# Optimization experiments

Hardware: AMD Instinct MI355X
Metric: run time of the kernel (lower is better)

The kernel has to match this reference:

```python
import jax, jax.numpy as jnp
import numpy as np

BIG = 1e30
B, Hh, Ww, DM = 8, 64, 64, 128
DI = 2 * DM          # d_inner
RR = -(-DM // 16)    # dt_rank = ceil(DM/16)
HID = 512


def _ln(x, g, b, eps):
    mu = jnp.mean(x, -1, keepdims=True)
    var = jnp.mean((x - mu) ** 2, -1, keepdims=True)
    return (x - mu) * jax.lax.rsqrt(var + eps) * g + b


def _silu(x):
    return x * jax.nn.sigmoid(x)


def _grid_weights(f):
    # f: [D,H,W]; MST edge weights exp(-cosine_sim) on 4-connected grid, BIG = invalid
    def cos(a, b):
        num = jnp.sum(a * b, 0)
        den = jnp.maximum(jnp.linalg.norm(a, axis=0) * jnp.linalg.norm(b, axis=0), 1e-8)
        return num / den
    wr = jnp.pad(jnp.exp(-cos(f[:, :, :-1], f[:, :, 1:])), ((0, 0), (0, 1)), constant_values=BIG).reshape(-1)
    wd = jnp.pad(jnp.exp(-cos(f[:, :-1, :], f[:, 1:, :])), ((0, 1), (0, 0)), constant_values=BIG).reshape(-1)
    return wr, wd


def _mst(wr, wd, H, W):
    # Prim's minimum spanning tree on HxW grid. Addition order is a valid
    # topological order (parent precedes child), equivalent to the BFS sort
    # for the order-invariant tree-scan aggregation.
    L = H * W

    def body(t, st):
        dist, par, intree, order = st
        v = jnp.argmin(jnp.where(intree, BIG, dist)).astype(jnp.int32)
        intree = intree.at[v].set(True)
        order = order.at[t].set(v)
        r, c = v // W, v % W
        for u, valid, w in (
            (v + 1, c < W - 1, wr[v]),
            (v - 1, c > 0, wr[jnp.clip(v - 1, 0, L - 1)]),
            (v + W, r < H - 1, wd[v]),
            (v - W, r > 0, wd[jnp.clip(v - W, 0, L - 1)]),
        ):
            uc = jnp.clip(u, 0, L - 1)
            better = valid & (~intree[uc]) & (w < dist[uc])
            dist = dist.at[uc].set(jnp.where(better, w, dist[uc]))
            par = par.at[uc].set(jnp.where(better, v, par[uc]))
        return dist, par, intree, order

    st0 = (jnp.full((L,), BIG, jnp.float32).at[0].set(-1.0),
           jnp.zeros((L,), jnp.int32),
           jnp.zeros((L,), bool),
           jnp.zeros((L,), jnp.int32))
    _, par, _, order = jax.lax.fori_loop(0, L, body, st0)
    return order, par


def _tree_scan(feat, ew, order, par):
    # feat, ew: [D,L]. Two-pass tree filter: out[i] = sum_j prod_{e in path(i,j)} w_e * f[j]
    vs = order[1:]
    ps = par[vs]

    def up_step(up, vp):
        v, p = vp
        return up.at[:, p].add(ew[:, v] * up[:, v]), None

    up, _ = jax.lax.scan(up_step, feat, (vs[::-1], ps[::-1]))
    root = order[0]
    out0 = jnp.zeros_like(up).at[:, root].set(up[:, root])

    def down_step(out, vp):
        v, p = vp
        w = ew[:, v]
        return out.at[:, v].set(up[:, v] + w * (out[:, p] - w * up[:, v])), None

    out, _ = jax.lax.scan(down_step, out0, (vs, ps))
    return out


def reference(x, ln1_g, ln1_b, ln2_g, ln2_b, w_in, conv_w, x_weight, dt_weight,
              dt_bias, a_logs, ds, hn_g, hn_b, on_g, on_b, w_out,
              mlp_w1, mlp_b1, mlp_w2, mlp_b2):
    Bb, H, W, _ = x.shape
    L = H * W
    # --- TreeScan branch ---
    h = _ln(x, ln1_g, ln1_b, 1e-6)
    xc, z = jnp.split(h @ w_in.T, 2, -1)
    z = _silu(z)
    xc = jnp.transpose(xc, (0, 3, 1, 2))                      # [B,Di,H,W]
    xc = _silu(jax.lax.conv_general_dilated(
        xc, conv_w, (1, 1), ((1, 1), (1, 1)),
        dimension_numbers=('NCHW', 'OIHW', 'NCHW'),
        feature_group_count=xc.shape[1]))
    Di = xc.shape[1]
    xs = xc.reshape(Bb, Di, L)
    R = dt_weight.shape[2]
    x_dbl = jnp.einsum('bdl,cd->bcl', xs, x_weight[0])        # [B,R+2,L]
    dts, Bs, Cs = x_dbl[:, :R], x_dbl[:, R:R + 1], x_dbl[:, R + 1:]
    dts = jnp.einsum('brl,dr->bdl', dts, dt_weight[0])
    dts = jax.nn.softplus(dts + dt_bias.reshape(-1)[None, :, None])
    As = -jnp.exp(a_logs.reshape(-1).astype(jnp.float32))     # N=1
    deltaA = jnp.exp(dts * As[None, :, None])                 # per-channel edge weights
    feat_in = dts * Bs * xs                                   # deltaB * x (K=N=1)
    # MST + topological sort under no-grad (matches torch.no_grad())
    f4t = jax.lax.stop_gradient(xs).reshape(Bb, Di, H, W)
    wr, wd = jax.vmap(_grid_weights)(f4t)
    order, par = jax.vmap(lambda a, b: _mst(a, b, H, W))(wr, wd)
    feat_out = jax.vmap(_tree_scan)(feat_in, deltaA, order, par)  # [B,Di,L]
    ho = _ln(jnp.swapaxes(feat_out, 1, 2), hn_g, hn_b, 1e-5)      # h_norm
    y = jnp.swapaxes(ho * jnp.swapaxes(Cs, 1, 2), 1, 2)           # multiply by Cs (N=1)
    y = y + ds[None, :, None] * xs                                # D skip
    y = _ln(jnp.swapaxes(y, 1, 2), on_g, on_b, 1e-5).reshape(Bb, H, W, Di)
    scan_out = (y * z) @ w_out.T
    # --- residual + MLP ---
    x1 = x + scan_out
    h2 = _ln(x1, ln2_g, ln2_b, 1e-6)
    mlp = jax.nn.gelu(h2 @ mlp_w1.T + mlp_b1) @ mlp_w2.T + mlp_b2
    return x1 + mlp


def setup_inputs():
    key = jax.random.key(0)
    ks = jax.random.split(key, 12)

    def rn(k, shape, s):
        return jax.random.normal(k, shape, jnp.float32) * s

    dt = jnp.exp(jax.random.uniform(ks[10], (DI,)) * (np.log(0.1) - np.log(0.001)) + np.log(0.001))
    dt_bias = (dt + jnp.log(-jnp.expm1(-dt)))[None]  # inverse-softplus init
    return {
        'x': rn(ks[0], (B, Hh, Ww, DM), 1.0),
        'ln1_g': jnp.ones((DM,)), 'ln1_b': jnp.zeros((DM,)),
        'ln2_g': jnp.ones((DM,)), 'ln2_b': jnp.zeros((DM,)),
        'w_in': rn(ks[1], (2 * DI, DM), DM ** -0.5),
        'conv_w': rn(ks[2], (DI, 1, 3, 3), 1.0 / 3.0),
        'x_weight': rn(ks[3], (1, RR + 2, DI), DI ** -0.5),
        'dt_weight': rn(ks[4], (1, DI, RR), RR ** -0.5),
        'dt_bias': dt_bias,
        'a_logs': jnp.zeros((DI, 1)),
        'ds': jnp.ones((DI,)),
        'hn_g': jnp.ones((DI,)), 'hn_b': jnp.zeros((DI,)),
        'on_g': jnp.ones((DI,)), 'on_b': jnp.zeros((DI,)),
        'w_out': rn(ks[5], (DM, DI), DI ** -0.5),
        'mlp_w1': rn(ks[6], (HID, DM), DM ** -0.5),
        'mlp_b1': jnp.zeros((HID,)),
        'mlp_w2': rn(ks[7], (DM, HID), HID ** -0.5),
        'mlp_b2': jnp.zeros((DM,)),
    }
```

## Files before the change

### kernel.cpp

```cpp
#include <hip/hip_runtime.h>
#include <hip/hip_bf16.h>
#include <cstdint>

#define BIGF 1e30f
constexpr int LB   = 4096;
constexpr int NB   = 8;
constexpr int MROWS = NB * LB;
constexpr int LSP  = 4104;

__device__ __forceinline__ float warp_sum(float v) {
#pragma unroll
  for (int off = 32; off; off >>= 1) v += __shfl_xor(v, off);
  return v;
}

__device__ __forceinline__ float block_sum256(float v) {
  __shared__ float sm[4];
  v = warp_sum(v);
  __syncthreads();
  if ((threadIdx.x & 63) == 0) sm[threadIdx.x >> 6] = v;
  __syncthreads();
  return sm[0] + sm[1] + sm[2] + sm[3];
}

__global__ __launch_bounds__(256) void ln128_kernel(
    const float* __restrict__ X, const float* __restrict__ g,
    const float* __restrict__ bb, float* __restrict__ O, float eps) {
  int wave = threadIdx.x >> 6, lane = threadIdx.x & 63;
  int row = blockIdx.x * 4 + wave;
  const float* xr = X + (size_t)row * 128;
  float x0 = xr[lane], x1 = xr[lane + 64];
  float mu = warp_sum(x0 + x1) * (1.0f / 128.0f);
  float d0 = x0 - mu, d1 = x1 - mu;
  float var = warp_sum(d0 * d0 + d1 * d1) * (1.0f / 128.0f);
  float s = 1.0f / sqrtf(var + eps);
  float* orow = O + (size_t)row * 128;
  orow[lane]      = d0 * s * g[lane]      + bb[lane];
  orow[lane + 64] = d1 * s * g[lane + 64] + bb[lane + 64];
}

template<int EPI>
__global__ __launch_bounds__(256) void gemm_kernel(
    const float* __restrict__ A, const float* __restrict__ W,
    float* __restrict__ C, float* __restrict__ C2,
    const float* __restrict__ bias, const float* __restrict__ addsrc,
    int M, int N, int K) {
  __shared__ float As[32][68];
  __shared__ float Bs[32][68];
  int t = threadIdx.x;
  int tx = t & 15, ty = t >> 4;
  int bm = blockIdx.y * 64, bn = blockIdx.x * 64;
  float acc[4][4] = {};
  for (int k0 = 0; k0 < K; k0 += 32) {
#pragma unroll
    for (int hh = 0; hh < 2; ++hh) {
      int q = t + hh * 256;
      int r = q >> 3, kc = q & 7;
      float4 a4 = reinterpret_cast<const float4*>(A + (size_t)(bm + r) * K + k0)[kc];
      float4 b4 = reinterpret_cast<const float4*>(W + (size_t)(bn + r) * K + k0)[kc];
      As[kc * 4 + 0][r] = a4.x; As[kc * 4 + 1][r] = a4.y;
      As[kc * 4 + 2][r] = a4.z; As[kc * 4 + 3][r] = a4.w;
      Bs[kc * 4 + 0][r] = b4.x; Bs[kc * 4 + 1][r] = b4.y;
      Bs[kc * 4 + 2][r] = b4.z; Bs[kc * 4 + 3][r] = b4.w;
    }
    __syncthreads();
#pragma unroll
    for (int kk = 0; kk < 32; ++kk) {
      float4 av = *reinterpret_cast<const float4*>(&As[kk][ty * 4]);
      float4 bv = *reinterpret_cast<const float4*>(&Bs[kk][tx * 4]);
      float aa[4] = {av.x, av.y, av.z, av.w};
      float bbv[4] = {bv.x, bv.y, bv.z, bv.w};
#pragma unroll
      for (int i = 0; i < 4; ++i)
#pragma unroll
        for (int j = 0; j < 4; ++j) acc[i][j] += aa[i] * bbv[j];
    }
    __syncthreads();
  }
#pragma unroll
  for (int i = 0; i < 4; ++i) {
    int m = bm + ty * 4 + i;
#pragma unroll
    for (int j = 0; j < 4; ++j) {
      int n = bn + tx * 4 + j;
      float v = acc[i][j];
      if (EPI == 1) {
        if (n < 256) C[(size_t)m * 256 + n] = v;
        else C2[(size_t)m * 256 + (n - 256)] = v / (1.0f + expf(-v));
      } else if (EPI == 2) {
        C[(size_t)m * N + n] = v + addsrc[(size_t)m * N + n];
      } else if (EPI == 3) {
        float u = v + bias[n];
        C[(size_t)m * N + n] =
            0.5f * u * (1.0f + tanhf(0.7978845608028654f * (u + 0.044715f * u * u * u)));
      } else if (EPI == 4) {
        C[(size_t)m * N + n] = v + bias[n] + addsrc[(size_t)m * N + n];
      }
    }
  }
}

__global__ __launch_bounds__(256) void convfeat_kernel(
    const float* __restrict__ xcpre, const float* __restrict__ cw,
    const float* __restrict__ xw, const float* __restrict__ dtw,
    const float* __restrict__ dtb, const float* __restrict__ alogs,
    float* __restrict__ xs, float* __restrict__ dAt, float* __restrict__ featt,
    float* __restrict__ Cs, float* __restrict__ ssq) {
  int m = blockIdx.x;
  int d = threadIdx.x;
  int l = m & (LB - 1), b = m >> 12;
  int r = l >> 6, c = l & 63;
  float acc = 0.f;
#pragma unroll
  for (int ky = 0; ky < 3; ++ky) {
    int rr = r + ky - 1;
    if (rr < 0 || rr > 63) continue;
#pragma unroll
    for (int kx = 0; kx < 3; ++kx) {
      int cc = c + kx - 1;
      if (cc < 0 || cc > 63) continue;
      int ml = (b << 12) + (rr << 6) + cc;
      acc += xcpre[(size_t)ml * 256 + d] * cw[d * 9 + ky * 3 + kx];
    }
  }
  float xv = acc / (1.0f + expf(-acc));
  xs[(size_t)m * 256 + d] = xv;
  float p[11];
#pragma unroll
  for (int i = 0; i < 10; ++i) p[i] = xv * xw[i * 256 + d];
  p[10] = xv * xv;
  __shared__ float sm[4][11];
#pragma unroll
  for (int i = 0; i < 11; ++i) p[i] = warp_sum(p[i]);
  int wv = d >> 6;
  if ((d & 63) == 0) {
    for (int i = 0; i < 11; ++i) sm[wv][i] = p[i];
  }
  __syncthreads();
  float red[11];
#pragma unroll
  for (int i = 0; i < 11; ++i) red[i] = sm[0][i] + sm[1][i] + sm[2][i] + sm[3][i];
  float xdt = dtb[d];
#pragma unroll
  for (int rr2 = 0; rr2 < 8; ++rr2) xdt += red[rr2] * dtw[d * 8 + rr2];
  float sp = fmaxf(xdt, 0.f) + log1pf(expf(-fabsf(xdt)));
  float As_ = -expf(alogs[d]);
  size_t tidx = ((size_t)(b * 64 + (d >> 2)) * 4096 + l) * 4 + (d & 3);
  dAt[tidx]   = expf(sp * As_);
  featt[tidx] = sp * red[8] * xv;
  if (d == 0) { Cs[m] = red[9]; ssq[m] = red[10]; }
}

__global__ __launch_bounds__(256) void gridw_kernel(
    const float* __restrict__ xs, const float* __restrict__ ssq,
    float* __restrict__ wrg, float* __restrict__ wdg) {
  int m = blockIdx.x, d = threadIdx.x;
  int l = m & (LB - 1);
  int r = l >> 6, c = l & 63;
  float a = xs[(size_t)m * 256 + d];
  float br = (c < 63) ? xs[(size_t)(m + 1) * 256 + d] : 0.f;
  float bd = (r < 63) ? xs[(size_t)(m + 64) * 256 + d] : 0.f;
  float s1 = warp_sum(a * br);
  float s2 = warp_sum(a * bd);
  __shared__ float sm[4][2];
  int wv = d >> 6;
  if ((d & 63) == 0) { sm[wv][0] = s1; sm[wv][1] = s2; }
  __syncthreads();
  if (d == 0) {
    float dotr = sm[0][0] + sm[1][0] + sm[2][0] + sm[3][0];
    float dotd = sm[0][1] + sm[1][1] + sm[2][1] + sm[3][1];
    float na = sqrtf(ssq[m]);
    float wrv = BIGF, wdv = BIGF;
    if (c < 63) { float den = fmaxf(na * sqrtf(ssq[m + 1]), 1e-8f);  wrv = expf(-(dotr / den)); }
    if (r < 63) { float den = fmaxf(na * sqrtf(ssq[m + 64]), 1e-8f); wdv = expf(-(dotd / den)); }
    wrg[m] = wrv; wdg[m] = wdv;
  }
}

__global__ __launch_bounds__(1024) void mst_kernel(
    const float* __restrict__ wr_g, const float* __restrict__ wd_g,
    unsigned short* __restrict__ levn16_g, unsigned short* __restrict__ parn16_g,
    int* __restrict__ levs_g) {
  __shared__ int pool[24592];
  __shared__ unsigned char flagR[4096];
  __shared__ unsigned char flagD[4096];
  __shared__ int ncomp_s;
  __shared__ int wred[16];
  int b = blockIdx.x, tid = threadIdx.x;
  float* wrs = (float*)pool;
  float* wds = (float*)(pool + 4096);
  int* comp = pool + 8192;
  int* lnk  = pool + 12288;
  unsigned int* bestw = (unsigned int*)(pool + 16384);
  int* beste = pool + 20480;
  const float* wrb = wr_g + b * 4096;
  const float* wdb = wd_g + b * 4096;
  for (int k = 0; k < 4; ++k) {
    int i = tid + k * 1024;
    wrs[i] = wrb[i]; wds[i] = wdb[i];
    comp[i] = i; flagR[i] = 0; flagD[i] = 0;
  }
  __syncthreads();
  for (int phase = 0; phase < 13; ++phase) {
    for (int k = 0; k < 4; ++k) {
      int c = tid + k * 1024;
      bestw[c] = 0xFFFFFFFFu; beste[c] = 0x7FFFFFFF; lnk[c] = c;
    }
    if (tid == 0) ncomp_s = 0;
    __syncthreads();
    for (int k = 0; k < 8; ++k) {
      int e = tid + k * 1024;
      int v = e & 4095;
      bool isR = e < 4096;
      int c = v & 63, r = v >> 6;
      bool valid = isR ? (c < 63) : (r < 63);
      if (valid) {
        int u = isR ? v + 1 : v + 64;
        int ca = comp[v], cb = comp[u];
        if (ca != cb) {
          unsigned wbits = __float_as_uint(isR ? wrs[v] : wds[v]);
          atomicMin(&bestw[ca], wbits);
          atomicMin(&bestw[cb], wbits);
        }
      }
    }
    __syncthreads();
    for (int k = 0; k < 8; ++k) {
      int e = tid + k * 1024;
      int v = e & 4095;
      bool isR = e < 4096;
      int c = v & 63, r = v >> 6;
      bool valid = isR ? (c < 63) : (r < 63);
      if (valid) {
        int u = isR ? v + 1 : v + 64;
        int ca = comp[v], cb = comp[u];
        if (ca != cb) {
          unsigned wbits = __float_as_uint(isR ? wrs[v] : wds[v]);
          if (wbits == bestw[ca]) atomicMin(&beste[ca], e);
          if (wbits == bestw[cb]) atomicMin(&beste[cb], e);
        }
      }
    }
    __syncthreads();
    for (int k = 0; k < 4; ++k) {
      int cc = tid + k * 1024;
      int e = beste[cc];
      if (e != 0x7FFFFFFF) {
        int v = e & 4095;
        bool isR = e < 4096;
        int u = isR ? v + 1 : v + 64;
        if (isR) flagR[v] = 1; else flagD[v] = 1;
        int ca = comp[v], cb = comp[u];
        lnk[cc] = (ca == cc) ? cb : ca;
      }
    }
    __syncthreads();
    for (int k = 0; k < 4; ++k) {
      int cc = tid + k * 1024;
      int l = lnk[cc];
      if (l != cc && lnk[l] == cc && cc < l) lnk[cc] = cc;
    }
    __syncthreads();
    for (int it = 0; it < 12; ++it) {
      for (int k = 0; k < 4; ++k) {
        int cc = tid + k * 1024;
        lnk[cc] = lnk[lnk[cc]];
      }
      __syncthreads();
    }
    for (int k = 0; k < 4; ++k) {
      int i = tid + k * 1024;
      comp[i] = lnk[comp[i]];
      if (comp[i] == i) atomicAdd(&ncomp_s, 1);
    }
    __syncthreads();
    if (ncomp_s <= 1) break;
    __syncthreads();
  }
  unsigned short* nxt = (unsigned short*)pool;
  short*          dsv = (short*)(pool + 8200);
  int* par = pool + 16400;
  int* dep = pool + 20496;
  const int NIL = 16384;
  unsigned short rn[16];
  int rd[16];
  int validm = 0;
  for (int k = 0; k < 4; ++k) { int i = tid + k * 1024; par[i] = 0; dep[i] = 0; }
#pragma unroll
  for (int k = 0; k < 16; ++k) {
    int a = tid + k * 1024;
    int u = a >> 2, d = a & 3;
    int c = u & 63, r = u >> 6;
    int mu = 0;
    if (r > 0  && flagD[u - 64]) mu |= 1;
    if (c > 0  && flagR[u - 1])  mu |= 2;
    if (c < 63 && flagR[u])      mu |= 4;
    if (r < 63 && flagD[u])      mu |= 8;
    unsigned short nx = NIL; short dv = 0;
    if (mu & (1 << d)) {
      validm |= 1 << k;
      int v = u + ((d == 0) ? -64 : (d == 1) ? -1 : (d == 2) ? 1 : 64);
      int cv = v & 63, rv = v >> 6;
      int mv = 0;
      if (rv > 0  && flagD[v - 64]) mv |= 1;
      if (cv > 0  && flagR[v - 1])  mv |= 2;
      if (cv < 63 && flagR[v])      mv |= 4;
      if (rv < 63 && flagD[v])      mv |= 8;
      int din = 3 - d;
      int hi = mv >> (din + 1);
      int dn = hi ? (din + __ffs(hi)) : (__ffs(mv) - 1);
      int nxv = v * 4 + dn;
      int m0 = (flagR[0] ? 4 : 0) | (flagD[0] ? 8 : 0);
      int a0 = __ffs(m0) - 1;
      if (v == 0 && nxv == a0) nxv = NIL;
      nx = (unsigned short)nxv;
      dv = 1;
    }
    nxt[a] = nx; dsv[a] = dv;
    rn[k] = nx; rd[k] = dv;
  }
  if (tid == 0) { nxt[NIL] = NIL; dsv[NIL] = 0; }
  __syncthreads();
#pragma unroll 1
  for (int it = 0; it < 13; ++it) {
    unsigned short nn[16]; short nd[16];
#pragma unroll
    for (int k = 0; k < 16; ++k) { nn[k] = nxt[rn[k]]; nd[k] = dsv[rn[k]]; }
    __syncthreads();
#pragma unroll
    for (int k = 0; k < 16; ++k) {
      int a = tid + k * 1024;
      rd[k] += nd[k];
      rn[k] = nn[k];
      nxt[a] = rn[k]; dsv[a] = (short)rd[k];
    }
    __syncthreads();
  }
#pragma unroll
  for (int k = 0; k < 16; ++k) if (validm & (1 << k)) {
    int a = tid + k * 1024;
    int u = a >> 2, d = a & 3;
    int v = u + ((d == 0) ? -64 : (d == 1) ? -1 : (d == 2) ? 1 : 64);
    int rb = v * 4 + (3 - d);
    if (rd[k] > (int)dsv[rb]) par[v] = u;
  }
  __syncthreads();
#pragma unroll
  for (int k = 0; k < 16; ++k) {
    int a = tid + k * 1024;
    int u = a >> 2, d = a & 3;
    unsigned short nx = NIL; short dv = 0;
    if (validm & (1 << k)) {
      int v = u + ((d == 0) ? -64 : (d == 1) ? -1 : (d == 2) ? 1 : 64);
      int cv = v & 63, rv = v >> 6;
      int mv = 0;
      if (rv > 0  && flagD[v - 64]) mv |= 1;
      if (cv > 0  && flagR[v - 1])  mv |= 2;
      if (cv < 63 && flagR[v])      mv |= 4;
      if (rv < 63 && flagD[v])      mv |= 8;
      int din = 3 - d;
      int hi = mv >> (din + 1);
      int dn = hi ? (din + __ffs(hi)) : (__ffs(mv) - 1);
      int nxv = v * 4 + dn;
      int m0 = (flagR[0] ? 4 : 0) | (flagD[0] ? 8 : 0);
      int a0 = __ffs(m0) - 1;
      if (v == 0 && nxv == a0) nxv = NIL;
      nx = (unsigned short)nxv;
      dv = (par[v] == u) ? (short)1 : (short)-1;
    }
    nxt[a] = nx; dsv[a] = dv;
    rn[k] = nx; rd[k] = dv;
  }
  __syncthreads();
#pragma unroll 1
  for (int it = 0; it < 13; ++it) {
    unsigned short nn[16]; short nd[16];
#pragma unroll
    for (int k = 0; k < 16; ++k) { nn[k] = nxt[rn[k]]; nd[k] = dsv[rn[k]]; }
    __syncthreads();
#pragma unroll
    for (int k = 0; k < 16; ++k) {
      int a = tid + k * 1024;
      rd[k] += nd[k];
      rn[k] = nn[k];
      nxt[a] = rn[k]; dsv[a] = (short)rd[k];
    }
    __syncthreads();
  }
#pragma unroll
  for (int k = 0; k < 16; ++k) if (validm & (1 << k)) {
    int a = tid + k * 1024;
    int u = a >> 2, d = a & 3;
    int v = u + ((d == 0) ? -64 : (d == 1) ? -1 : (d == 2) ? 1 : 64);
    if (par[v] == u) dep[v] = 1 - rd[k];
  }
  __syncthreads();
  int md = 0;
  for (int k = 0; k < 4; ++k) md = max(md, dep[tid + k * 1024]);
#pragma unroll
  for (int off = 32; off; off >>= 1) md = max(md, __shfl_xor(md, off));
  if ((tid & 63) == 0) wred[tid >> 6] = md;
  __syncthreads();
  if (tid == 0) {
    int m = 0;
    for (int i = 0; i < 16; ++i) m = max(m, wred[i]);
    wred[0] = m;
  }
  __syncthreads();
  int maxd = wred[0];
  __syncthreads();
  int* cnt  = pool;
  int* offs = pool + 4096;
  for (int k = 0; k < 4; ++k) cnt[tid + k * 1024] = 0;
  __syncthreads();
  for (int k = 0; k < 4; ++k) atomicAdd(&cnt[dep[tid + k * 1024]], 1);
  __syncthreads();
  int base4 = tid * 4;
  int c0 = cnt[base4], c1 = cnt[base4 + 1], c2 = cnt[base4 + 2], c3 = cnt[base4 + 3];
  int tsum = c0 + c1 + c2 + c3;
  int lane = tid & 63, wid = tid >> 6;
  int iv = tsum;
  for (int off = 1; off < 64; off <<= 1) {
    int n = __shfl_up(iv, off);
    if (lane >= off) iv += n;
  }
  if (lane == 63) wred[wid] = iv;
  __syncthreads();
  if (tid == 0) {
    int acc = 0;
    for (int i = 0; i < 16; ++i) { int t = wred[i]; wred[i] = acc; acc += t; }
  }
  __syncthreads();
  int excl = iv - tsum + wred[wid];
  offs[base4]     = excl;
  offs[base4 + 1] = excl + c0;
  offs[base4 + 2] = excl + c0 + c1;
  offs[base4 + 3] = excl + c0 + c1 + c2;
  __syncthreads();
  for (int idx = tid; idx <= maxd; idx += 1024) levs_g[b * LSP + idx] = offs[idx];
  if (tid == 0) {
    levs_g[b * LSP + maxd + 1] = 4096;
    levs_g[b * LSP + 4098] = maxd + 1;
  }
  __syncthreads();
  for (int k = 0; k < 4; ++k) {
    int v2 = tid + k * 1024;
    int pos = atomicAdd(&offs[dep[v2]], 1);
    int c = v2 & 63, r = v2 >> 6;
    unsigned msk = 0;
    if (r > 0  && par[v2 - 64] == v2) msk |= 1;
    if (c > 0  && par[v2 - 1]  == v2) msk |= 2;
    if (c < 63 && par[v2 + 1]  == v2) msk |= 4;
    if (r < 63 && par[v2 + 64] == v2) msk |= 8;
    levn16_g[b * 4096 + pos] = (unsigned short)(v2 | (msk << 12));
    parn16_g[b * 4096 + pos] = (unsigned short)par[v2];
  }
}

__global__ __launch_bounds__(64) void scan_kernel(
    float* __restrict__ buft, const float* __restrict__ ewt,
    const unsigned short* __restrict__ levn16_g,
    const unsigned short* __restrict__ parn16_g,
    const int* __restrict__ levs_g) {
  __shared__ float pr[32776];
  __shared__ unsigned int topo[4096];
  __shared__ unsigned short lvs[4104];
  int bid = blockIdx.x;
  int b = bid >> 6;
  int cg = bid & 63;
  int lane = threadIdx.x;
  int nlev = levs_g[b * LSP + 4098];
  size_t tbase = (size_t)(b * 64 + cg) * 4096;
  float2* pr2 = reinterpret_cast<float2*>(pr);
  const float4* bt4 = reinterpret_cast<const float4*>(buft) + tbase;
  const float4* et4 = reinterpret_cast<const float4*>(ewt) + tbase;
  for (int n = lane; n < 4096; n += 64) {
    float4 bv = bt4[n];
    float4 ev = et4[n];
    pr2[0 * 4097 + n] = make_float2(bv.x, ev.x);
    pr2[1 * 4097 + n] = make_float2(bv.y, ev.y);
    pr2[2 * 4097 + n] = make_float2(bv.z, ev.z);
    pr2[3 * 4097 + n] = make_float2(bv.w, ev.w);
  }
  const unsigned int* lv32 = reinterpret_cast<const unsigned int*>(levn16_g + b * 4096);
  const unsigned int* pn32 = reinterpret_cast<const unsigned int*>(parn16_g + b * 4096);
  for (int i2 = lane; i2 < 2048; i2 += 64) {
    unsigned int a = lv32[i2], p = pn32[i2];
    topo[2 * i2]     = (a & 0xFFFFu) | (p << 16);
    topo[2 * i2 + 1] = (a >> 16) | (p & 0xFFFF0000u);
  }
  for (int i = lane; i <= nlev; i += 64) lvs[i] = (unsigned short)levs_g[b * LSP + i];
  __syncthreads();
  int ch = lane & 3;
  int slot = lane >> 2;
  int cpl = ch * 4097;
  if (nlev > 1) {
    int s = lvs[nlev - 1], e = lvs[nlev];
    int jn = s + slot;
    unsigned int pkn = topo[jn & 4095];
    for (int lev = nlev - 1; lev >= 1; --lev) {
      int ce = e;
      int j = jn;
      unsigned int pk = pkn;
      if (lev > 1) {
        e = s; s = lvs[lev - 1];
        jn = s + slot;
        pkn = topo[jn & 4095];
      }
      bool first = true;
      while (j < ce) {
        if (!first) pk = topo[j];
        first = false;
        int v = pk & 4095;
        int p = (pk >> 16) & 4095;
        float2 self = pr2[cpl + v];
        atomicAdd(&pr[(cpl + p) * 2], self.y * self.x);
        j += 16;
      }
      __builtin_amdgcn_wave_barrier();
    }
  }
  __builtin_amdgcn_wave_barrier();
  if (nlev > 1) {
    int s = lvs[1], e = lvs[2];
    int jn = s + slot;
    unsigned int pkn = topo[jn & 4095];
    for (int lev = 1; lev < nlev; ++lev) {
      int ce = e;
      int j = jn;
      unsigned int pk = pkn;
      if (lev + 1 < nlev) {
        s = e; e = lvs[lev + 2];
        jn = s + slot;
        pkn = topo[jn & 4095];
      }
      bool first = true;
      while (j < ce) {
        if (!first) pk = topo[j];
        first = false;
        int v = pk & 4095;
        int p = (pk >> 16) & 4095;
        float2 self = pr2[cpl + v];
        float pb = pr[(cpl + p) * 2];
        float w = self.y, uv = self.x;
        pr[(cpl + v) * 2] = uv + w * (pb - w * uv);
        j += 16;
      }
      __builtin_amdgcn_wave_barrier();
    }
  }
  __syncthreads();
  float4* bw4 = reinterpret_cast<float4*>(buft) + tbase;
  for (int n = lane; n < 4096; n += 64) {
    float2 c0 = pr2[0 * 4097 + n];
    float2 c1 = pr2[1 * 4097 + n];
    float2 c2 = pr2[2 * 4097 + n];
    float2 c3 = pr2[3 * 4097 + n];
    bw4[n] = make_float4(c0.x, c1.x, c2.x, c3.x);
  }
}

__global__ __launch_bounds__(256) void post_kernel(
    const float* __restrict__ buft, const float* __restrict__ Cs,
    const float* __restrict__ xs, const float* __restrict__ ds,
    const float* __restrict__ hng, const float* __restrict__ hnb,
    const float* __restrict__ ong, const float* __restrict__ onb,
    float* __restrict__ zya) {
  int m = blockIdx.x, d = threadIdx.x;
  int b = m >> 12, l = m & (LB - 1);
  size_t idx = (size_t)m * 256 + d;
  float fo = buft[((size_t)(b * 64 + (d >> 2)) * 4096 + l) * 4 + (d & 3)];
  float mu = block_sum256(fo) * (1.f / 256.f);
  float dv = fo - mu;
  float var = block_sum256(dv * dv) * (1.f / 256.f);
  float ho = dv * (1.0f / sqrtf(var + 1e-5f)) * hng[d] + hnb[d];
  float y = ho * Cs[m] + ds[d] * xs[idx];
  float mu2 = block_sum256(y) * (1.f / 256.f);
  float dy = y - mu2;
  float var2 = block_sum256(dy * dy) * (1.f / 256.f);
  float y2 = dy * (1.0f / sqrtf(var2 + 1e-5f)) * ong[d] + onb[d];
  zya[idx] = y2 * zya[idx];
}

extern "C" void kernel_launch(void* const* d_in, const int* in_sizes, int n_in,
                              void* d_out, int out_size, void* d_ws, size_t ws_size,
                              hipStream_t stream) {
  (void)in_sizes; (void)n_in; (void)out_size; (void)ws_size;
  const float* x      = (const float*)d_in[0];
  const float* ln1g   = (const float*)d_in[1];
  const float* ln1b   = (const float*)d_in[2];
  const float* ln2g   = (const float*)d_in[3];
  const float* ln2b   = (const float*)d_in[4];
  const float* w_in   = (const float*)d_in[5];
  const float* conv_w = (const float*)d_in[6];
  const float* xw     = (const float*)d_in[7];
  const float* dtw    = (const float*)d_in[8];
  const float* dtb    = (const float*)d_in[9];
  const float* alogs  = (const float*)d_in[10];
  const float* dsv    = (const float*)d_in[11];
  const float* hng    = (const float*)d_in[12];
  const float* hnb    = (const float*)d_in[13];
  const float* ong    = (const float*)d_in[14];
  const float* onb    = (const float*)d_in[15];
  const float* w_out  = (const float*)d_in[16];
  const float* mw1    = (const float*)d_in[17];
  const float* mb1    = (const float*)d_in[18];
  const float* mw2    = (const float*)d_in[19];
  const float* mb2    = (const float*)d_in[20];

  char* ws = (char*)d_ws;
  float* h    = (float*)(ws + 0);
  float* z    = (float*)(ws + 16777216);
  float* xcp  = (float*)(ws + 50331648);
  float* xs   = (float*)(ws + 83886080);
  float* dAt  = (float*)(ws + 117440512);
  float* featt= (float*)(ws + 150994944);
  float* Cs   = (float*)(ws + 184549376);
  float* ssq  = (float*)(ws + 184680448);
  float* wr   = (float*)(ws + 184811520);
  float* wd   = (float*)(ws + 184942592);
  unsigned short* levn16 = (unsigned short*)(ws + 185073664);
  unsigned short* parn16 = (unsigned short*)(ws + 185204736);
  int*   levs = (int*)(ws + 185335808);
  float* midg = xs;
  float* x1   = h;
  float* h2   = xcp;

  ln128_kernel<<<MROWS / 4, 256, 0, stream>>>(x, ln1g, ln1b, h, 1e-6f);
  gemm_kernel<1><<<dim3(8, 512), 256, 0, stream>>>(h, w_in, xcp, z, nullptr, nullptr,
                                                   MROWS, 512, 128);
  convfeat_kernel<<<MROWS, 256, 0, stream>>>(xcp, conv_w, xw, dtw, dtb, alogs,
                                             xs, dAt, featt, Cs, ssq);
  gridw_kernel<<<MROWS, 256, 0, stream>>>(xs, ssq, wr, wd);
  mst_kernel<<<NB, 1024, 0, stream>>>(wr, wd, levn16, parn16, levs);
  scan_kernel<<<512, 64, 0, stream>>>(featt, dAt, levn16, parn16, levs);
  post_kernel<<<MROWS, 256, 0, stream>>>(featt, Cs, xs, dsv, hng, hnb, ong, onb, z);
  gemm_kernel<2><<<dim3(2, 512), 256, 0, stream>>>(z, w_out, x1, nullptr, nullptr, x,
                                                   MROWS, 128, 256);
  ln128_kernel<<<MROWS / 4, 256, 0, stream>>>(x1, ln2g, ln2b, h2, 1e-6f);
  gemm_kernel<3><<<dim3(8, 512), 256, 0, stream>>>(h2, mw1, midg, nullptr, mb1, nullptr,
                                                   MROWS, 512, 128);
  gemm_kernel<4><<<dim3(2, 512), 256, 0, stream>>>(midg, mw2, (float*)d_out, nullptr,
                                                   mb2, x1, MROWS, 128, 512);
}
```

Measured before the change: 874.4 us.

## Add 128x128 GEMM tile, fast-math intrinsics, packed topo, and restructured tree scan

Result: faster. 841.0 us (-3.8%).

```diff
diff --git a/kernel.cpp b/kernel.cpp
--- a/kernel.cpp
+++ b/kernel.cpp
@@ -84,17 +84,68 @@
     for (int j = 0; j < 4; ++j) {
       int n = bn + tx * 4 + j;
       float v = acc[i][j];
+      if (EPI == 2) {
+        C[(size_t)m * N + n] = v + addsrc[(size_t)m * N + n];
+      } else if (EPI == 4) {
+        C[(size_t)m * N + n] = v + bias[n] + addsrc[(size_t)m * N + n];
+      }
+    }
+  }
+}
+
+template<int EPI>
+__global__ __launch_bounds__(256) void gemm128_kernel(
+    const float* __restrict__ A, const float* __restrict__ W,
+    float* __restrict__ C, float* __restrict__ C2,
+    const float* __restrict__ bias, int M, int N, int K) {
+  __shared__ float As[32][132];
+  __shared__ float Bs[32][132];
+  int t = threadIdx.x;
+  int tx = t & 15, ty = t >> 4;
+  int bm = blockIdx.y * 128, bn = blockIdx.x * 128;
+  float acc[8][8] = {};
+  for (int k0 = 0; k0 < K; k0 += 32) {
+#pragma unroll
+    for (int hh = 0; hh < 4; ++hh) {
+      int q = t + hh * 256;
+      int r = q >> 3, kc = q & 7;
+      float4 a4 = *reinterpret_cast<const float4*>(A + (size_t)(bm + r) * K + k0 + kc * 4);
+      float4 b4 = *reinterpret_cast<const float4*>(W + (size_t)(bn + r) * K + k0 + kc * 4);
+      As[kc * 4 + 0][r] = a4.x; As[kc * 4 + 1][r] = a4.y;
+      As[kc * 4 + 2][r] = a4.z; As[kc * 4 + 3][r] = a4.w;
+      Bs[kc * 4 + 0][r] = b4.x; Bs[kc * 4 + 1][r] = b4.y;
+      Bs[kc * 4 + 2][r] = b4.z; Bs[kc * 4 + 3][r] = b4.w;
+    }
+    __syncthreads();
+#pragma unroll
+    for (int kk = 0; kk < 32; ++kk) {
+      float4 a0 = *reinterpret_cast<const float4*>(&As[kk][ty * 4]);
+      float4 a1 = *reinterpret_cast<const float4*>(&As[kk][64 + ty * 4]);
+      float4 b0 = *reinterpret_cast<const float4*>(&Bs[kk][tx * 4]);
+      float4 b1 = *reinterpret_cast<const float4*>(&Bs[kk][64 + tx * 4]);
+      float aa[8] = {a0.x, a0.y, a0.z, a0.w, a1.x, a1.y, a1.z, a1.w};
+      float bb2[8] = {b0.x, b0.y, b0.z, b0.w, b1.x, b1.y, b1.z, b1.w};
+#pragma unroll
+      for (int i = 0; i < 8; ++i)
+#pragma unroll
+        for (int j = 0; j < 8; ++j) acc[i][j] += aa[i] * bb2[j];
+    }
+    __syncthreads();
+  }
+#pragma unroll
+  for (int i = 0; i < 8; ++i) {
+    int m = bm + (i >> 2) * 64 + ty * 4 + (i & 3);
+#pragma unroll
+    for (int j = 0; j < 8; ++j) {
+      int n = bn + (j >> 2) * 64 + tx * 4 + (j & 3);
+      float v = acc[i][j];
       if (EPI == 1) {
         if (n < 256) C[(size_t)m * 256 + n] = v;
-        else C2[(size_t)m * 256 + (n - 256)] = v / (1.0f + expf(-v));
-      } else if (EPI == 2) {
-        C[(size_t)m * N + n] = v + addsrc[(size_t)m * N + n];
+        else C2[(size_t)m * 256 + (n - 256)] = v / (1.0f + __expf(-v));
       } else if (EPI == 3) {
         float u = v + bias[n];
-        C[(size_t)m * N + n] =
-            0.5f * u * (1.0f + tanhf(0.7978845608028654f * (u + 0.044715f * u * u * u)));
-      } else if (EPI == 4) {
-        C[(size_t)m * N + n] = v + bias[n] + addsrc[(size_t)m * N + n];
+        float xg = 1.5957691216057308f * (u + 0.044715f * u * u * u);
+        C[(size_t)m * N + n] = u / (1.0f + __expf(-xg));
       }
     }
   }
@@ -123,7 +174,7 @@
       acc += xcpre[(size_t)ml * 256 + d] * cw[d * 9 + ky * 3 + kx];
     }
   }
-  float xv = acc / (1.0f + expf(-acc));
+  float xv = acc / (1.0f + __expf(-acc));
   xs[(size_t)m * 256 + d] = xv;
   float p[11];
 #pragma unroll
@@ -143,10 +194,10 @@
   float xdt = dtb[d];
 #pragma unroll
   for (int rr2 = 0; rr2 < 8; ++rr2) xdt += red[rr2] * dtw[d * 8 + rr2];
-  float sp = fmaxf(xdt, 0.f) + log1pf(expf(-fabsf(xdt)));
-  float As_ = -expf(alogs[d]);
+  float sp = fmaxf(xdt, 0.f) + __logf(1.0f + __expf(-fabsf(xdt)));
+  float As_ = -__expf(alogs[d]);
   size_t tidx = ((size_t)(b * 64 + (d >> 2)) * 4096 + l) * 4 + (d & 3);
-  dAt[tidx]   = expf(sp * As_);
+  dAt[tidx]   = __expf(sp * As_);
   featt[tidx] = sp * red[8] * xv;
   if (d == 0) { Cs[m] = red[9]; ssq[m] = red[10]; }
 }
@@ -179,8 +230,7 @@
 
 __global__ __launch_bounds__(1024) void mst_kernel(
     const float* __restrict__ wr_g, const float* __restrict__ wd_g,
-    unsigned short* __restrict__ levn16_g, unsigned short* __restrict__ parn16_g,
-    int* __restrict__ levs_g) {
+    unsigned int* __restrict__ topo_g, int* __restrict__ levs_g) {
   __shared__ int pool[24592];
   __shared__ unsigned char flagR[4096];
   __shared__ unsigned char flagD[4096];
@@ -452,112 +502,109 @@
     if (c > 0  && par[v2 - 1]  == v2) msk |= 2;
     if (c < 63 && par[v2 + 1]  == v2) msk |= 4;
     if (r < 63 && par[v2 + 64] == v2) msk |= 8;
-    levn16_g[b * 4096 + pos] = (unsigned short)(v2 | (msk << 12));
-    parn16_g[b * 4096 + pos] = (unsigned short)par[v2];
+    topo_g[b * 4096 + pos] =
+        (unsigned)v2 | (msk << 12) | ((unsigned)par[v2] << 16);
   }
 }
 
 __global__ __launch_bounds__(64) void scan_kernel(
     float* __restrict__ buft, const float* __restrict__ ewt,
-    const unsigned short* __restrict__ levn16_g,
-    const unsigned short* __restrict__ parn16_g,
-    const int* __restrict__ levs_g) {
-  __shared__ float pr[32776];
-  __shared__ unsigned int topo[4096];
+    const unsigned int* __restrict__ topo_g, const int* __restrict__ levs_g) {
+  __shared__ float acc[16384];
   __shared__ unsigned short lvs[4104];
   int bid = blockIdx.x;
-  int b = bid >> 6;
-  int cg = bid & 63;
+  int b = bid >> 6, cg = bid & 63;
   int lane = threadIdx.x;
+  int ch = lane & 3, slot = lane >> 2;
   int nlev = levs_g[b * LSP + 4098];
-  size_t tbase = (size_t)(b * 64 + cg) * 4096;
-  float2* pr2 = reinterpret_cast<float2*>(pr);
-  const float4* bt4 = reinterpret_cast<const float4*>(buft) + tbase;
-  const float4* et4 = reinterpret_cast<const float4*>(ewt) + tbase;
+  size_t fbase = (size_t)(b * 64 + cg) * 16384;
+  const float4* bt4 = reinterpret_cast<const float4*>(buft + fbase);
+  const float*  ewf = ewt + fbase;
+  const float4* et4 = reinterpret_cast<const float4*>(ewf);
+  const unsigned int* tp = topo_g + b * 4096;
+  float4* acc4 = reinterpret_cast<float4*>(acc);
+  float wsum = 0.f;
   for (int n = lane; n < 4096; n += 64) {
-    float4 bv = bt4[n];
+    acc4[n] = bt4[n];
     float4 ev = et4[n];
-    pr2[0 * 4097 + n] = make_float2(bv.x, ev.x);
-    pr2[1 * 4097 + n] = make_float2(bv.y, ev.y);
-    pr2[2 * 4097 + n] = make_float2(bv.z, ev.z);
-    pr2[3 * 4097 + n] = make_float2(bv.w, ev.w);
-  }
-  const unsigned int* lv32 = reinterpret_cast<const unsigned int*>(levn16_g + b * 4096);
-  const unsigned int* pn32 = reinterpret_cast<const unsigned int*>(parn16_g + b * 4096);
-  for (int i2 = lane; i2 < 2048; i2 += 64) {
-    unsigned int a = lv32[i2], p = pn32[i2];
-    topo[2 * i2]     = (a & 0xFFFFu) | (p << 16);
-    topo[2 * i2 + 1] = (a >> 16) | (p & 0xFFFF0000u);
-  }
+    wsum += ev.x + ev.y + ev.z + ev.w;
+  }
+  asm volatile("" :: "v"(wsum));
   for (int i = lane; i <= nlev; i += 64) lvs[i] = (unsigned short)levs_g[b * LSP + i];
   __syncthreads();
-  int ch = lane & 3;
-  int slot = lane >> 2;
-  int cpl = ch * 4097;
   if (nlev > 1) {
-    int s = lvs[nlev - 1], e = lvs[nlev];
-    int jn = s + slot;
-    unsigned int pkn = topo[jn & 4095];
+    int sA = lvs[nlev - 1], eA = lvs[nlev];
+    int jA = sA + slot;
+    unsigned tAv = tp[jA < 4096 ? jA : 4095];
+    int vA = tAv & 4095, pA = (tAv >> 16) & 4095;
+    float elA = ewf[vA * 4 + ch];
+    int sB = 0, eB = 0, jB = 0; unsigned tBv = 0;
+    if (nlev - 2 >= 1) { sB = lvs[nlev - 2]; eB = sA; jB = sB + slot; tBv = tp[jB < 4096 ? jB : 4095]; }
     for (int lev = nlev - 1; lev >= 1; --lev) {
-      int ce = e;
-      int j = jn;
-      unsigned int pk = pkn;
-      if (lev > 1) {
-        e = s; s = lvs[lev - 1];
-        jn = s + slot;
-        pkn = topo[jn & 4095];
-      }
-      bool first = true;
-      while (j < ce) {
-        if (!first) pk = topo[j];
-        first = false;
-        int v = pk & 4095;
-        int p = (pk >> 16) & 4095;
-        float2 self = pr2[cpl + v];
-        atomicAdd(&pr[(cpl + p) * 2], self.y * self.x);
-        j += 16;
+      int vB = tBv & 4095, pB = (tBv >> 16) & 4095;
+      float elB = 0.f;
+      if (lev - 1 >= 1) elB = ewf[vB * 4 + ch];
+      int sC = 0, jC = 0; unsigned tCv = 0;
+      if (lev - 2 >= 1) { sC = lvs[lev - 2]; jC = sC + slot; tCv = tp[jC < 4096 ? jC : 4095]; }
+      if (jA < eA) {
+        float a = acc[vA * 4 + ch];
+        atomicAdd(&acc[pA * 4 + ch], elA * a);
+        for (int j = jA + 16; j < eA; j += 16) {
+          unsigned t = tp[j];
+          int v = t & 4095, p = (t >> 16) & 4095;
+          float e = ewf[v * 4 + ch];
+          float av = acc[v * 4 + ch];
+          atomicAdd(&acc[p * 4 + ch], e * av);
+        }
       }
       __builtin_amdgcn_wave_barrier();
+      int oldsB = sB;
+      vA = vB; pA = pB; elA = elB; jA = jB; eA = eB; sA = oldsB;
+      sB = sC; eB = oldsB; jB = jC; tBv = tCv;
     }
   }
   __builtin_amdgcn_wave_barrier();
   if (nlev > 1) {
-    int s = lvs[1], e = lvs[2];
-    int jn = s + slot;
-    unsigned int pkn = topo[jn & 4095];
+    int sA = lvs[1], eA = lvs[2];
+    int jA = sA + slot;
+    unsigned tAv = tp[jA < 4096 ? jA : 4095];
+    int vA = tAv & 4095, pA = (tAv >> 16) & 4095;
+    float elA = ewf[vA * 4 + ch];
+    float uvA = acc[vA * 4 + ch];
+    int sB = 0, eB = 0, jB = 0; unsigned tBv = 0;
+    if (nlev > 2) { sB = eA; eB = lvs[3 <= nlev ? 3 : nlev]; jB = sB + slot; tBv = tp[jB < 4096 ? jB : 4095]; }
     for (int lev = 1; lev < nlev; ++lev) {
-      int ce = e;
-      int j = jn;
-      unsigned int pk = pkn;
+      int vB = tBv & 4095, pB = (tBv >> 16) & 4095;
+      float elB = 0.f, uvB = 0.f;
       if (lev + 1 < nlev) {
-        s = e; e = lvs[lev + 2];
-        jn = s + slot;
-        pkn = topo[jn & 4095];
-      }
-      bool first = true;
-      while (j < ce) {
-        if (!first) pk = topo[j];
-        first = false;
-        int v = pk & 4095;
-        int p = (pk >> 16) & 4095;
-        float2 self = pr2[cpl + v];
-        float pb = pr[(cpl + p) * 2];
-        float w = self.y, uv = self.x;
-        pr[(cpl + v) * 2] = uv + w * (pb - w * uv);
-        j += 16;
+        elB = ewf[vB * 4 + ch];
+        uvB = acc[vB * 4 + ch];
+      }
+      int sC = 0, eC = 0, jC = 0; unsigned tCv = 0;
+      if (lev + 2 < nlev) {
+        sC = lvs[lev + 2]; eC = lvs[lev + 3];
+        jC = sC + slot; tCv = tp[jC < 4096 ? jC : 4095];
+      }
+      if (jA < eA) {
+        float pb = acc[pA * 4 + ch];
+        acc[vA * 4 + ch] = uvA + elA * (pb - elA * uvA);
+        for (int j = jA + 16; j < eA; j += 16) {
+          unsigned t = tp[j];
+          int v = t & 4095, p = (t >> 16) & 4095;
+          float e = ewf[v * 4 + ch];
+          float uv = acc[v * 4 + ch];
+          float pbv = acc[p * 4 + ch];
+          acc[v * 4 + ch] = uv + e * (pbv - e * uv);
+        }
       }
       __builtin_amdgcn_wave_barrier();
-    }
-  }
-  __syncthreads();
-  float4* bw4 = reinterpret_cast<float4*>(buft) + tbase;
-  for (int n = lane; n < 4096; n += 64) {
-    float2 c0 = pr2[0 * 4097 + n];
-    float2 c1 = pr2[1 * 4097 + n];
-    float2 c2 = pr2[2 * 4097 + n];
-    float2 c3 = pr2[3 * 4097 + n];
-    bw4[n] = make_float4(c0.x, c1.x, c2.x, c3.x);
-  }
+      vA = vB; pA = pB; elA = elB; uvA = uvB; jA = jB; sA = sB; eA = eB;
+      sB = sC; eB = eC; jB = jC; tBv = tCv;
+    }
+  }
+  __syncthreads();
+  float4* bw4 = reinterpret_cast<float4*>(buft + fbase);
+  for (int n = lane; n < 4096; n += 64) bw4[n] = acc4[n];
 }
 
 __global__ __launch_bounds__(256) void post_kernel(
@@ -619,27 +666,26 @@
   float* ssq  = (float*)(ws + 184680448);
   float* wr   = (float*)(ws + 184811520);
   float* wd   = (float*)(ws + 184942592);
-  unsigned short* levn16 = (unsigned short*)(ws + 185073664);
-  unsigned short* parn16 = (unsigned short*)(ws + 185204736);
+  unsigned int* topo32 = (unsigned int*)(ws + 185073664);
   int*   levs = (int*)(ws + 185335808);
   float* midg = xs;
   float* x1   = h;
   float* h2   = xcp;
 
   ln128_kernel<<<MROWS / 4, 256, 0, stream>>>(x, ln1g, ln1b, h, 1e-6f);
-  gemm_kernel<1><<<dim3(8, 512), 256, 0, stream>>>(h, w_in, xcp, z, nullptr, nullptr,
-                                                   MROWS, 512, 128);
+  gemm128_kernel<1><<<dim3(4, 256), 256, 0, stream>>>(h, w_in, xcp, z, nullptr,
+                                                      MROWS, 512, 128);
   convfeat_kernel<<<MROWS, 256, 0, stream>>>(xcp, conv_w, xw, dtw, dtb, alogs,
                                              xs, dAt, featt, Cs, ssq);
   gridw_kernel<<<MROWS, 256, 0, stream>>>(xs, ssq, wr, wd);
-  mst_kernel<<<NB, 1024, 0, stream>>>(wr, wd, levn16, parn16, levs);
-  scan_kernel<<<512, 64, 0, stream>>>(featt, dAt, levn16, parn16, levs);
+  mst_kernel<<<NB, 1024, 0, stream>>>(wr, wd, topo32, levs);
+  scan_kernel<<<512, 64, 0, stream>>>(featt, dAt, topo32, levs);
   post_kernel<<<MROWS, 256, 0, stream>>>(featt, Cs, xs, dsv, hng, hnb, ong, onb, z);
   gemm_kernel<2><<<dim3(2, 512), 256, 0, stream>>>(z, w_out, x1, nullptr, nullptr, x,
                                                    MROWS, 128, 256);
   ln128_kernel<<<MROWS / 4, 256, 0, stream>>>(x1, ln2g, ln2b, h2, 1e-6f);
-  gemm_kernel<3><<<dim3(8, 512), 256, 0, stream>>>(h2, mw1, midg, nullptr, mb1, nullptr,
-                                                   MROWS, 512, 128);
+  gemm128_kernel<3><<<dim3(4, 256), 256, 0, stream>>>(h2, mw1, midg, nullptr, mb1,
+                                                      MROWS, 512, 128);
   gemm_kernel<4><<<dim3(2, 512), 256, 0, stream>>>(midg, mw2, (float*)d_out, nullptr,
                                                    mb2, x1, MROWS, 128, 512);
 }
```
